# Optimization experiments

Hardware: AMD Instinct MI355X
Metric: run time of the kernel (lower is better)

Reference implementation:

```python
import jax, jax.numpy as jnp
import numpy as np

B, L, CH = 8, 32768, 128   # segments, points per segment, channels
H, D = 4, 32               # num_head, ch_head (CH == H*D)
EPS = 1e-5                 # torch GroupNorm default eps


def group_norm1(x, w, b):
    # GroupNorm(num_groups=1, num_channels=CH) applied on [1, CH, L] per segment:
    # normalize over all channels AND points of each segment, then per-channel affine.
    mu = jnp.mean(x, axis=(1, 2), keepdims=True)            # [B,1,1]
    var = jnp.var(x, axis=(1, 2), keepdims=True)            # [B,1,1]
    return (x - mu) * jax.lax.rsqrt(var + EPS) * w + b      # [B,L,CH]


def setup_inputs() -> dict:
    key = jax.random.key(0)
    k0, k1, k2 = jax.random.split(key, 3)
    x = jax.random.normal(k0, (B, L, CH), dtype=jnp.float32)
    W_qkv = jax.random.normal(k1, (CH, 3 * H * D), dtype=jnp.float32) * 0.02
    W_out = jax.random.normal(k2, (H * D, CH), dtype=jnp.float32) * 0.02
    gn1_w = jnp.ones((CH,), jnp.float32)
    gn1_b = jnp.zeros((CH,), jnp.float32)
    gn2_w = jnp.ones((CH,), jnp.float32)
    gn2_b = jnp.zeros((CH,), jnp.float32)
    return {"x": x, "gn1_w": gn1_w, "gn1_b": gn1_b, "W_qkv": W_qkv,
            "W_out": W_out, "gn2_w": gn2_w, "gn2_b": gn2_b}


def reference(x, gn1_w, gn1_b, W_qkv, W_out, gn2_w, gn2_b):
    norm_x = group_norm1(x, gn1_w, gn1_b)                     # [B,L,CH]
    qkv = norm_x @ W_qkv                                      # [B,L,3*H*D]
    q, k, v = jnp.split(qkv, 3, axis=-1)
    q = q.reshape(B, L, H, D)
    k = k.reshape(B, L, H, D)
    v = v.reshape(B, L, H, D)
    # softmax over points within each segment (k / sqrt(segment_len))
    k_soft = jax.nn.softmax(k * (1.0 / np.float32(np.sqrt(L))), axis=1)
    # per-segment, per-head KV context: [B,H,D,D]
    context = jnp.einsum('blhk,blhv->bhkv', k_soft, v)
    # q scaled by ch_head**-0.5, softmax over feature dim
    q_soft = jax.nn.softmax(q * np.float32(D ** -0.5), axis=-1)
    out = jnp.einsum('blhk,bhkv->blhv', q_soft, context).reshape(B, L, H * D)
    out = out @ W_out                                          # [B,L,CH]
    out = group_norm1(out, gn2_w, gn2_b)
    return out + x  # residual
```

## Files before the change

### kernel.cpp

```cpp
#include <hip/hip_runtime.h>

#define NSEG 8
#define LSEG 32768
#define NCH 128
#define EPS_GN 1e-5f
#define KSCALE 0.005524271728019903f
#define QSCALE 0.17677669529663687f

typedef __attribute__((ext_vector_type(4))) float f32x4;
typedef __attribute__((ext_vector_type(8))) __bf16 bf16x8;
typedef __attribute__((ext_vector_type(4))) short s16x4;

static __device__ __forceinline__ unsigned short f2bf(float f) {
  unsigned int u = __float_as_uint(f);
  u += 0x7fffu + ((u >> 16) & 1u);
  return (unsigned short)(u >> 16);
}
static __device__ __forceinline__ float bf2f(unsigned short s) {
  return __uint_as_float(((unsigned int)s) << 16);
}

__global__ void k_wcvt(const float* __restrict__ W, unsigned short* __restrict__ WT) {
  int idx = blockIdx.x * 256 + threadIdx.x;
  int n = idx >> 7, k = idx & 127;
  WT[idx] = f2bf(W[k * 384 + n]);
}

__global__ __launch_bounds__(256) void k_stats1(const float* __restrict__ x, float* __restrict__ part) {
  int t = threadIdx.x;
  int b = blockIdx.x >> 6, p = blockIdx.x & 63;
  const float4* xp = (const float4*)x + (size_t)b * 1048576 + (size_t)p * 16384;
  float s = 0.f, q = 0.f;
  for (int i = 0; i < 64; ++i) {
    float4 v = xp[t + i * 256];
    s += v.x + v.y + v.z + v.w;
    q += v.x*v.x + v.y*v.y + v.z*v.z + v.w*v.w;
  }
  #pragma unroll
  for (int o = 1; o < 64; o <<= 1) { s += __shfl_xor(s, o); q += __shfl_xor(q, o); }
  __shared__ float red[8];
  int wave = t >> 6, lane = t & 63;
  if (lane == 0) { red[wave*2] = s; red[wave*2+1] = q; }
  __syncthreads();
  if (t == 0) {
    part[blockIdx.x*2]   = red[0] + red[2] + red[4] + red[6];
    part[blockIdx.x*2+1] = red[1] + red[3] + red[5] + red[7];
  }
}

__global__ void k_stats1_final(const float* __restrict__ part, float* __restrict__ stats) {
  int b = blockIdx.x, t = threadIdx.x;
  float s = part[(b*64 + t)*2], q = part[(b*64 + t)*2 + 1];
  #pragma unroll
  for (int o = 1; o < 64; o <<= 1) { s += __shfl_xor(s, o); q += __shfl_xor(q, o); }
  if (t == 0) {
    const float invN = 1.f / 4194304.f;
    float mu = s * invN;
    float var = q * invN - mu * mu;
    stats[b*2] = mu;
    stats[b*2+1] = rsqrtf(var + EPS_GN);
  }
}

__global__ __launch_bounds__(512) void k_qkv(
    const float* __restrict__ x, const float* __restrict__ gn1w, const float* __restrict__ gn1b,
    const float* __restrict__ stats1, const unsigned short* __restrict__ WT,
    unsigned short* __restrict__ q_ws, float* __restrict__ sume_p, float* __restrict__ ctx_p)
{
  __shared__ __attribute__((aligned(16))) unsigned short sW[384 * 136];
  __shared__ __attribute__((aligned(16))) unsigned short sA[128 * 136];
  __shared__ float sume_lds[8 * 128];

  const int t = threadIdx.x;
  const int wave = t >> 6, lane = t & 63;
  const int b = blockIdx.x >> 5, sub = blockIdx.x & 31;
  const int lm = lane & 15, lg = lane >> 4;

  const ushort4* wt4 = (const ushort4*)WT;
  #pragma unroll
  for (int i = 0; i < 24; ++i) {
    int f = t + i * 512;
    *(ushort4*)&sW[(f >> 5) * 136 + (f & 31) * 4] = wt4[f];
  }

  const float mu = stats1[b*2], rs = stats1[b*2+1];
  const int c4 = t & 31;
  const float4 w4 = *(const float4*)&gn1w[c4*4];
  const float4 g4 = *(const float4*)&gn1b[c4*4];

  f32x4 ctx[4][2][2];
  #pragma unroll
  for (int h = 0; h < 4; ++h)
    #pragma unroll
    for (int i = 0; i < 2; ++i)
      #pragma unroll
      for (int j = 0; j < 2; ++j) ctx[h][i][j] = (f32x4){0.f,0.f,0.f,0.f};
  float se[8] = {0.f,0.f,0.f,0.f,0.f,0.f,0.f,0.f};

  const float4* xp = (const float4*)x + ((size_t)b * LSEG + (size_t)sub * 1024) * 32;
  ushort4* q4 = (ushort4*)q_ws;

  for (int ch = 0; ch < 8; ++ch) {
    #pragma unroll
    for (int i = 0; i < 8; ++i) {
      int f = t + i * 512;
      int row = f >> 5;
      float4 v = xp[ch * 4096 + f];
      float4 nv;
      nv.x = (v.x - mu) * rs * w4.x + g4.x;
      nv.y = (v.y - mu) * rs * w4.y + g4.y;
      nv.z = (v.z - mu) * rs * w4.z + g4.z;
      nv.w = (v.w - mu) * rs * w4.w + g4.w;
      *(ushort4*)&sA[row * 136 + c4 * 4] = make_ushort4(f2bf(nv.x), f2bf(nv.y), f2bf(nv.z), f2bf(nv.w));
    }
    __syncthreads();

    const int arow = wave * 16 + lm;
    bf16x8 af[4];
    #pragma unroll
    for (int kk = 0; kk < 4; ++kk)
      af[kk] = *(const bf16x8*)&sA[arow * 136 + kk * 32 + lg * 8];

    f32x4 qa[8];
    #pragma unroll
    for (int nt = 0; nt < 8; ++nt) qa[nt] = (f32x4){0.f,0.f,0.f,0.f};
    #pragma unroll
    for (int kk = 0; kk < 4; ++kk)
      #pragma unroll
      for (int nt = 0; nt < 8; ++nt) {
        bf16x8 bf = *(const bf16x8*)&sW[(nt * 16 + lm) * 136 + kk * 32 + lg * 8];
        qa[nt] = __builtin_amdgcn_mfma_f32_16x16x32_bf16(af[kk], bf, qa[nt], 0, 0, 0);
      }
    const size_t qbase = (((size_t)blockIdx.x * 8 + ch) * 8 + wave) * 8;
    #pragma unroll
    for (int nt = 0; nt < 8; ++nt)
      q4[(qbase + nt) * 64 + lane] =
          make_ushort4(f2bf(qa[nt][0]), f2bf(qa[nt][1]), f2bf(qa[nt][2]), f2bf(qa[nt][3]));

    f32x4 ka[8], va[8];
    #pragma unroll
    for (int j = 0; j < 8; ++j) { ka[j] = (f32x4){0.f,0.f,0.f,0.f}; va[j] = (f32x4){0.f,0.f,0.f,0.f}; }
    #pragma unroll
    for (int kk = 0; kk < 4; ++kk) {
      #pragma unroll
      for (int j = 0; j < 8; ++j) {
        bf16x8 bk = *(const bf16x8*)&sW[((8 + j) * 16 + lm) * 136 + kk * 32 + lg * 8];
        ka[j] = __builtin_amdgcn_mfma_f32_16x16x32_bf16(af[kk], bk, ka[j], 0, 0, 0);
      }
      #pragma unroll
      for (int j = 0; j < 8; ++j) {
        bf16x8 bv = *(const bf16x8*)&sW[((16 + j) * 16 + lm) * 136 + kk * 32 + lg * 8];
        va[j] = __builtin_amdgcn_mfma_f32_16x16x32_bf16(af[kk], bv, va[j], 0, 0, 0);
      }
    }
    #pragma unroll
    for (int j = 0; j < 8; ++j) {
      #pragma unroll
      for (int r = 0; r < 4; ++r) ka[j][r] = __expf(ka[j][r] * KSCALE);
      float s = ka[j][0] + ka[j][1] + ka[j][2] + ka[j][3];
      s += __shfl_xor(s, 16);
      s += __shfl_xor(s, 32);
      se[j] += s;
    }
    #pragma unroll
    for (int h = 0; h < 4; ++h) {
      s16x4 aE[2], bV[2];
      #pragma unroll
      for (int d = 0; d < 2; ++d) {
        #pragma unroll
        for (int r = 0; r < 4; ++r) {
          aE[d][r] = (short)f2bf(ka[2*h + d][r]);
          bV[d][r] = (short)f2bf(va[2*h + d][r]);
        }
      }
      #pragma unroll
      for (int dt = 0; dt < 2; ++dt)
        #pragma unroll
        for (int vt = 0; vt < 2; ++vt)
          ctx[h][dt][vt] = __builtin_amdgcn_mfma_f32_16x16x16bf16_1k(aE[dt], bV[vt], ctx[h][dt][vt], 0, 0, 0);
    }
    __syncthreads();
  }

  if (lane < 16) {
    #pragma unroll
    for (int j = 0; j < 8; ++j) sume_lds[wave * 128 + j * 16 + lane] = se[j];
  }
  __syncthreads();
  if (t < 128) {
    float s = 0.f;
    #pragma unroll
    for (int w = 0; w < 8; ++w) s += sume_lds[w * 128 + t];
    sume_p[(size_t)blockIdx.x * 128 + t] = s;
  }
  float* cbuf = (float*)sA;
  for (int w = 0; w < 8; ++w) {
    if (wave == w) {
      #pragma unroll
      for (int h = 0; h < 4; ++h)
        #pragma unroll
        for (int dt = 0; dt < 2; ++dt)
          #pragma unroll
          for (int vt = 0; vt < 2; ++vt)
            #pragma unroll
            for (int r = 0; r < 4; ++r) {
              int idx = (h * 32 + dt * 16 + lg * 4 + r) * 32 + vt * 16 + lm;
              if (w == 0) cbuf[idx] = ctx[h][dt][vt][r];
              else        cbuf[idx] += ctx[h][dt][vt][r];
            }
    }
    __syncthreads();
  }
  #pragma unroll
  for (int i = 0; i < 8; ++i) {
    int f = t + i * 512;
    ctx_p[(size_t)blockIdx.x * 4096 + f] = cbuf[f];
  }
}

__global__ __launch_bounds__(512) void k_ctx_final(
    const float* __restrict__ sume_p, const float* __restrict__ ctx_p,
    const float* __restrict__ Wout, unsigned short* __restrict__ WcT)
{
  __shared__ float sse[128];
  __shared__ float sctx[4096];
  __shared__ float sWo[16384];
  const int t = threadIdx.x, b = blockIdx.x;
  if (t < 128) {
    float s = 0.f;
    for (int blk = 0; blk < 32; ++blk) s += sume_p[(size_t)(b * 32 + blk) * 128 + t];
    sse[t] = s;
  }
  float cv[8];
  #pragma unroll
  for (int j = 0; j < 8; ++j) {
    int idx = t + j * 512;
    float s = 0.f;
    for (int blk = 0; blk < 32; ++blk) s += ctx_p[(size_t)(b * 32 + blk) * 4096 + idx];
    cv[j] = s;
  }
  #pragma unroll
  for (int j = 0; j < 32; ++j) sWo[t + j * 512] = Wout[t + j * 512];
  __syncthreads();
  #pragma unroll
  for (int j = 0; j < 8; ++j) {
    int idx = t + j * 512;
    sctx[idx] = cv[j] / sse[idx >> 5];
  }
  __syncthreads();
  const int p = t >> 2, c0 = (t & 3) * 32;
  const int h = p >> 5;
  float acc[32];
  #pragma unroll
  for (int j = 0; j < 32; ++j) acc[j] = 0.f;
  for (int v = 0; v < 32; ++v) {
    float a = sctx[p * 32 + v];
    const float* wr = &sWo[(h * 32 + v) * 128 + c0];
    #pragma unroll
    for (int j = 0; j < 32; ++j) acc[j] += a * wr[j];
  }
  #pragma unroll
  for (int j = 0; j < 32; ++j)
    WcT[((size_t)b * 128 + (c0 + j)) * 128 + p] = f2bf(acc[j]);
}

__global__ __launch_bounds__(512) void k_out(
    unsigned short* __restrict__ q_ws, const unsigned short* __restrict__ WcT,
    float* __restrict__ stats2_p)
{
  __shared__ __attribute__((aligned(16))) unsigned short sQ[128 * 136];
  __shared__ __attribute__((aligned(16))) unsigned short sWc[128 * 136];
  __shared__ __attribute__((aligned(16))) unsigned short sO[128 * 136];
  __shared__ float red[16];

  const int t = threadIdx.x;
  const int wave = t >> 6, lane = t & 63;
  const int b = blockIdx.x >> 5, sub = blockIdx.x & 31;
  const int lm = lane & 15, lg = lane >> 4;

  const ushort4* wc4 = (const ushort4*)WcT + (size_t)b * 4096;
  #pragma unroll
  for (int i = 0; i < 8; ++i) {
    int f = t + i * 512;
    *(ushort4*)&sWc[(f >> 5) * 136 + (f & 31) * 4] = wc4[f];
  }

  ushort4* q4 = (ushort4*)q_ws;
  float ssum = 0.f, ssq = 0.f;

  for (int ch = 0; ch < 8; ++ch) {
    const size_t qbase = (((size_t)blockIdx.x * 8 + ch) * 8 + wave) * 8;
    ushort4 qf[8];
    #pragma unroll
    for (int nt = 0; nt < 8; ++nt) qf[nt] = q4[(qbase + nt) * 64 + lane];
    const int rbase = wave * 16 + lg * 4;
    #pragma unroll
    for (int h = 0; h < 4; ++h) {
      float a0[4], a1[4], m[4], e0[4], e1[4], sm[4];
      a0[0] = bf2f(qf[2*h].x) * QSCALE;   a0[1] = bf2f(qf[2*h].y) * QSCALE;
      a0[2] = bf2f(qf[2*h].z) * QSCALE;   a0[3] = bf2f(qf[2*h].w) * QSCALE;
      a1[0] = bf2f(qf[2*h+1].x) * QSCALE; a1[1] = bf2f(qf[2*h+1].y) * QSCALE;
      a1[2] = bf2f(qf[2*h+1].z) * QSCALE; a1[3] = bf2f(qf[2*h+1].w) * QSCALE;
      #pragma unroll
      for (int r = 0; r < 4; ++r) m[r] = fmaxf(a0[r], a1[r]);
      #pragma unroll
      for (int o = 1; o < 16; o <<= 1)
        #pragma unroll
        for (int r = 0; r < 4; ++r) m[r] = fmaxf(m[r], __shfl_xor(m[r], o));
      #pragma unroll
      for (int r = 0; r < 4; ++r) {
        e0[r] = __expf(a0[r] - m[r]); e1[r] = __expf(a1[r] - m[r]); sm[r] = e0[r] + e1[r];
      }
      #pragma unroll
      for (int o = 1; o < 16; o <<= 1)
        #pragma unroll
        for (int r = 0; r < 4; ++r) sm[r] += __shfl_xor(sm[r], o);
      #pragma unroll
      for (int r = 0; r < 4; ++r) {
        float inv = 1.f / sm[r];
        sQ[(rbase + r) * 136 + h * 32 + lm]      = f2bf(e0[r] * inv);
        sQ[(rbase + r) * 136 + h * 32 + 16 + lm] = f2bf(e1[r] * inv);
      }
    }
    __syncthreads();
    const int arow = wave * 16 + lm;
    bf16x8 af[4];
    #pragma unroll
    for (int kk = 0; kk < 4; ++kk)
      af[kk] = *(const bf16x8*)&sQ[arow * 136 + kk * 32 + lg * 8];
    f32x4 acc[8];
    #pragma unroll
    for (int nt = 0; nt < 8; ++nt) acc[nt] = (f32x4){0.f,0.f,0.f,0.f};
    #pragma unroll
    for (int kk = 0; kk < 4; ++kk)
      #pragma unroll
      for (int nt = 0; nt < 8; ++nt) {
        bf16x8 bf = *(const bf16x8*)&sWc[(nt * 16 + lm) * 136 + kk * 32 + lg * 8];
        acc[nt] = __builtin_amdgcn_mfma_f32_16x16x32_bf16(af[kk], bf, acc[nt], 0, 0, 0);
      }
    #pragma unroll
    for (int nt = 0; nt < 8; ++nt)
      #pragma unroll
      for (int r = 0; r < 4; ++r) {
        float v = acc[nt][r];
        ssum += v; ssq += v * v;
        sO[(rbase + r) * 136 + nt * 16 + lm] = f2bf(v);
      }
    __syncthreads();
    const size_t rowg = (size_t)b * LSEG + (size_t)sub * 1024 + (size_t)ch * 128;
    #pragma unroll
    for (int i = 0; i < 8; ++i) {
      int f = t + i * 512;
      q4[(rowg + (f >> 5)) * 32 + (f & 31)] = *(const ushort4*)&sO[(f >> 5) * 136 + (f & 31) * 4];
    }
  }
  #pragma unroll
  for (int o = 1; o < 64; o <<= 1) { ssum += __shfl_xor(ssum, o); ssq += __shfl_xor(ssq, o); }
  if (lane == 0) { red[wave*2] = ssum; red[wave*2+1] = ssq; }
  __syncthreads();
  if (t == 0) {
    float s = 0.f, q = 0.f;
    #pragma unroll
    for (int w = 0; w < 8; ++w) { s += red[w*2]; q += red[w*2+1]; }
    stats2_p[blockIdx.x*2] = s; stats2_p[blockIdx.x*2+1] = q;
  }
}

__global__ void k_stats2_final(const float* __restrict__ part, float* __restrict__ stats) {
  int b = blockIdx.x, t = threadIdx.x;
  float s = part[(b*32 + t)*2], q = part[(b*32 + t)*2 + 1];
  #pragma unroll
  for (int o = 1; o < 32; o <<= 1) { s += __shfl_xor(s, o); q += __shfl_xor(q, o); }
  if (t == 0) {
    const float invN = 1.f / 4194304.f;
    float mu = s * invN;
    float var = q * invN - mu * mu;
    stats[b*2] = mu;
    stats[b*2+1] = rsqrtf(var + EPS_GN);
  }
}

__global__ __launch_bounds__(256) void k_final(
    const float* __restrict__ x, const unsigned short* __restrict__ out_ws,
    const float* __restrict__ stats2, const float* __restrict__ gn2w, const float* __restrict__ gn2b,
    float* __restrict__ y)
{
  const int t = threadIdx.x;
  const int b = blockIdx.x >> 8, blk = blockIdx.x & 255;
  const float mu = stats2[b*2], rs = stats2[b*2+1];
  const int c4 = t & 31;
  const float4 w4 = *(const float4*)&gn2w[c4*4];
  const float4 g4 = *(const float4*)&gn2b[c4*4];
  const size_t base = (size_t)b * 1048576 + (size_t)blk * 4096;
  const float4* xp = (const float4*)x + base;
  const ushort4* op = (const ushort4*)out_ws + base;
  float4* yp = (float4*)y + base;
  #pragma unroll
  for (int i = 0; i < 16; ++i) {
    int f = t + i * 256;
    float4 xv = xp[f];
    ushort4 ov = op[f];
    float4 r;
    r.x = (bf2f(ov.x) - mu) * rs * w4.x + g4.x + xv.x;
    r.y = (bf2f(ov.y) - mu) * rs * w4.y + g4.y + xv.y;
    r.z = (bf2f(ov.z) - mu) * rs * w4.z + g4.z + xv.z;
    r.w = (bf2f(ov.w) - mu) * rs * w4.w + g4.w + xv.w;
    yp[f] = r;
  }
}

extern "C" void kernel_launch(void* const* d_in, const int* in_sizes, int n_in,
                              void* d_out, int out_size, void* d_ws, size_t ws_size,
                              hipStream_t stream) {
  const float* x    = (const float*)d_in[0];
  const float* gn1w = (const float*)d_in[1];
  const float* gn1b = (const float*)d_in[2];
  const float* Wqkv = (const float*)d_in[3];
  const float* Wout = (const float*)d_in[4];
  const float* gn2w = (const float*)d_in[5];
  const float* gn2b = (const float*)d_in[6];
  float* y = (float*)d_out;
  char* ws = (char*)d_ws;

  float*          stats1p = (float*)(ws + 0);
  float*          stats1  = (float*)(ws + 4096);
  unsigned short* WT      = (unsigned short*)(ws + 8192);
  float*          sume_p  = (float*)(ws + 106496);
  float*          ctx_p   = (float*)(ws + 237568);
  unsigned short* WcT     = (unsigned short*)(ws + 4431872);
  float*          stats2p = (float*)(ws + 4694016);
  float*          stats2  = (float*)(ws + 4696064);
  unsigned short* q_ws    = (unsigned short*)(ws + 4718592);

  hipLaunchKernelGGL(k_wcvt,         dim3(192),  dim3(256), 0, stream, Wqkv, WT);
  hipLaunchKernelGGL(k_stats1,       dim3(512),  dim3(256), 0, stream, x, stats1p);
  hipLaunchKernelGGL(k_stats1_final, dim3(8),    dim3(64),  0, stream, stats1p, stats1);
  hipLaunchKernelGGL(k_qkv,          dim3(256),  dim3(512), 0, stream, x, gn1w, gn1b, stats1, WT, q_ws, sume_p, ctx_p);
  hipLaunchKernelGGL(k_ctx_final,    dim3(8),    dim3(512), 0, stream, sume_p, ctx_p, Wout, WcT);
  hipLaunchKernelGGL(k_out,          dim3(256),  dim3(512), 0, stream, q_ws, WcT, stats2p);
  hipLaunchKernelGGL(k_stats2_final, dim3(8),    dim3(32),  0, stream, stats2p, stats2);
  hipLaunchKernelGGL(k_final,        dim3(2048), dim3(256), 0, stream, x, q_ws, stats2, gn2w, gn2b, y);
}
```

Baseline: 238.1 us.

## Fold GroupNorm1 into QKV weights and bias, restructure qkv and out kernels

```diff
diff --git a/kernel.cpp b/kernel.cpp
--- a/kernel.cpp
+++ b/kernel.cpp
@@ -2,7 +2,6 @@
 
 #define NSEG 8
 #define LSEG 32768
-#define NCH 128
 #define EPS_GN 1e-5f
 #define KSCALE 0.005524271728019903f
 #define QSCALE 0.17677669529663687f
@@ -19,11 +18,28 @@
 static __device__ __forceinline__ float bf2f(unsigned short s) {
   return __uint_as_float(((unsigned int)s) << 16);
 }
-
-__global__ void k_wcvt(const float* __restrict__ W, unsigned short* __restrict__ WT) {
+static __device__ __forceinline__ bf16x8 cvt8(float4 a, float4 b) {
+  bf16x8 r;
+  r[0] = (__bf16)a.x; r[1] = (__bf16)a.y; r[2] = (__bf16)a.z; r[3] = (__bf16)a.w;
+  r[4] = (__bf16)b.x; r[5] = (__bf16)b.y; r[6] = (__bf16)b.z; r[7] = (__bf16)b.w;
+  return r;
+}
+static __device__ __forceinline__ s16x4 pack4(float a, float b, float c, float d) {
+  union { __bf16 h[4]; s16x4 s; } u;
+  u.h[0] = (__bf16)a; u.h[1] = (__bf16)b; u.h[2] = (__bf16)c; u.h[3] = (__bf16)d;
+  return u.s;
+}
+static __device__ __forceinline__ ushort4 packu4(f32x4 v) {
+  union { __bf16 h[4]; ushort4 u; } u;
+  u.h[0] = (__bf16)v[0]; u.h[1] = (__bf16)v[1]; u.h[2] = (__bf16)v[2]; u.h[3] = (__bf16)v[3];
+  return u.u;
+}
+
+__global__ void k_wcvt(const float* __restrict__ W, const float* __restrict__ gn1w,
+                       unsigned short* __restrict__ WT) {
   int idx = blockIdx.x * 256 + threadIdx.x;
-  int n = idx >> 7, k = idx & 127;
-  WT[idx] = f2bf(W[k * 384 + n]);
+  int n = idx >> 7, ch = idx & 127;
+  WT[idx] = f2bf(gn1w[ch] * W[ch * 384 + n]);
 }
 
 __global__ __launch_bounds__(256) void k_stats1(const float* __restrict__ x, float* __restrict__ part) {
@@ -62,159 +78,152 @@
   }
 }
 
-__global__ __launch_bounds__(512) void k_qkv(
-    const float* __restrict__ x, const float* __restrict__ gn1w, const float* __restrict__ gn1b,
-    const float* __restrict__ stats1, const unsigned short* __restrict__ WT,
+__global__ void k_bias(const float* __restrict__ Wqkv, const float* __restrict__ gn1w,
+                       const float* __restrict__ gn1b, const float* __restrict__ stats1,
+                       float* __restrict__ biasv, float* __restrict__ alpha) {
+  int seg = blockIdx.x, n = threadIdx.x;
+  float mu = stats1[seg*2], rs = stats1[seg*2+1];
+  float s = 0.f;
+  for (int ch = 0; ch < 128; ++ch)
+    s += (gn1b[ch] - mu * rs * gn1w[ch]) * Wqkv[ch * 384 + n];
+  float scale = (n < 128) ? QSCALE : ((n < 256) ? KSCALE : 1.f);
+  biasv[seg*384 + n] = s * scale;
+  if (n == 0) {
+    alpha[seg*4]   = rs * QSCALE;
+    alpha[seg*4+1] = rs * KSCALE;
+    alpha[seg*4+2] = rs;
+  }
+}
+
+__global__ __launch_bounds__(512, 2) void k_qkv(
+    const float* __restrict__ x, const unsigned short* __restrict__ WT,
+    const float* __restrict__ biasv, const float* __restrict__ alpha,
     unsigned short* __restrict__ q_ws, float* __restrict__ sume_p, float* __restrict__ ctx_p)
 {
-  __shared__ __attribute__((aligned(16))) unsigned short sW[384 * 136];
-  __shared__ __attribute__((aligned(16))) unsigned short sA[128 * 136];
-  __shared__ float sume_lds[8 * 128];
+  __shared__ float cbuf[4096];
+  __shared__ float sume_lds[256];
 
   const int t = threadIdx.x;
   const int wave = t >> 6, lane = t & 63;
-  const int b = blockIdx.x >> 5, sub = blockIdx.x & 31;
+  const int rg = wave >> 2, h = wave & 3;
   const int lm = lane & 15, lg = lane >> 4;
-
-  const ushort4* wt4 = (const ushort4*)WT;
-  #pragma unroll
-  for (int i = 0; i < 24; ++i) {
-    int f = t + i * 512;
-    *(ushort4*)&sW[(f >> 5) * 136 + (f & 31) * 4] = wt4[f];
-  }
-
-  const float mu = stats1[b*2], rs = stats1[b*2+1];
-  const int c4 = t & 31;
-  const float4 w4 = *(const float4*)&gn1w[c4*4];
-  const float4 g4 = *(const float4*)&gn1b[c4*4];
-
-  f32x4 ctx[4][2][2];
-  #pragma unroll
-  for (int h = 0; h < 4; ++h)
-    #pragma unroll
-    for (int i = 0; i < 2; ++i)
-      #pragma unroll
-      for (int j = 0; j < 2; ++j) ctx[h][i][j] = (f32x4){0.f,0.f,0.f,0.f};
-  float se[8] = {0.f,0.f,0.f,0.f,0.f,0.f,0.f,0.f};
-
-  const float4* xp = (const float4*)x + ((size_t)b * LSEG + (size_t)sub * 1024) * 32;
+  const int bid = blockIdx.x;
+  const int seg = bid >> 5, sub = bid & 31;
+
+  bf16x8 wq[2][4], wk[2][4], wv[2][4];
+  #pragma unroll
+  for (int nt = 0; nt < 2; ++nt)
+    #pragma unroll
+    for (int kk = 0; kk < 4; ++kk) {
+      int row = h*32 + nt*16 + lm;
+      wq[nt][kk] = *(const bf16x8*)&WT[(row      ) * 128 + kk*32 + lg*8];
+      wk[nt][kk] = *(const bf16x8*)&WT[(row + 128) * 128 + kk*32 + lg*8];
+      wv[nt][kk] = *(const bf16x8*)&WT[(row + 256) * 128 + kk*32 + lg*8];
+    }
+  const float alk = alpha[seg*4 + 1];
+  const float alv = alpha[seg*4 + 2];
+  float ckv[2], cvv[2];
+  #pragma unroll
+  for (int nt = 0; nt < 2; ++nt) {
+    ckv[nt] = biasv[seg*384 + 128 + h*32 + nt*16 + lm];
+    cvv[nt] = biasv[seg*384 + 256 + h*32 + nt*16 + lm];
+  }
+
+  f32x4 ctx00 = {0,0,0,0}, ctx01 = {0,0,0,0}, ctx10 = {0,0,0,0}, ctx11 = {0,0,0,0};
+  float se0 = 0.f, se1 = 0.f;
+
+  const float* xw = x + ((size_t)seg * LSEG + sub*1024 + rg*64 + lm) * 128 + lg*8;
   ushort4* q4 = (ushort4*)q_ws;
 
-  for (int ch = 0; ch < 8; ++ch) {
-    #pragma unroll
-    for (int i = 0; i < 8; ++i) {
-      int f = t + i * 512;
-      int row = f >> 5;
-      float4 v = xp[ch * 4096 + f];
-      float4 nv;
-      nv.x = (v.x - mu) * rs * w4.x + g4.x;
-      nv.y = (v.y - mu) * rs * w4.y + g4.y;
-      nv.z = (v.z - mu) * rs * w4.z + g4.z;
-      nv.w = (v.w - mu) * rs * w4.w + g4.w;
-      *(ushort4*)&sA[row * 136 + c4 * 4] = make_ushort4(f2bf(nv.x), f2bf(nv.y), f2bf(nv.z), f2bf(nv.w));
+#define ISSUE(S, IT) { \
+    const float* p_ = xw + (size_t)((((IT) >> 2) * 128) + (((IT) & 3) * 16)) * 128; \
+    _Pragma("unroll") \
+    for (int kk = 0; kk < 4; ++kk) { \
+      S[kk][0] = *(const float4*)(p_ + kk*32); \
+      S[kk][1] = *(const float4*)(p_ + kk*32 + 4); \
+    } }
+
+#define COMPUTE(S, IT) { \
+    bf16x8 axf[4]; \
+    _Pragma("unroll") for (int kk = 0; kk < 4; ++kk) axf[kk] = cvt8(S[kk][0], S[kk][1]); \
+    f32x4 qa0 = {0,0,0,0}, qa1 = {0,0,0,0}; \
+    _Pragma("unroll") for (int kk = 0; kk < 4; ++kk) { \
+      qa0 = __builtin_amdgcn_mfma_f32_16x16x32_bf16(wq[0][kk], axf[kk], qa0, 0, 0, 0); \
+      qa1 = __builtin_amdgcn_mfma_f32_16x16x32_bf16(wq[1][kk], axf[kk], qa1, 0, 0, 0); \
+    } \
+    { size_t T_ = ((size_t)bid*8 + ((IT) >> 2)) * 64 + (rg*4 + ((IT) & 3)) * 8 + h*2; \
+      q4[(T_    ) * 64 + lane] = packu4(qa0); \
+      q4[(T_ + 1) * 64 + lane] = packu4(qa1); } \
+    f32x4 ka0 = {0,0,0,0}, ka1 = {0,0,0,0}; \
+    _Pragma("unroll") for (int kk = 0; kk < 4; ++kk) { \
+      ka0 = __builtin_amdgcn_mfma_f32_16x16x32_bf16(axf[kk], wk[0][kk], ka0, 0, 0, 0); \
+      ka1 = __builtin_amdgcn_mfma_f32_16x16x32_bf16(axf[kk], wk[1][kk], ka1, 0, 0, 0); \
+    } \
+    f32x4 va0 = {0,0,0,0}, va1 = {0,0,0,0}; \
+    _Pragma("unroll") for (int kk = 0; kk < 4; ++kk) { \
+      va0 = __builtin_amdgcn_mfma_f32_16x16x32_bf16(axf[kk], wv[0][kk], va0, 0, 0, 0); \
+      va1 = __builtin_amdgcn_mfma_f32_16x16x32_bf16(axf[kk], wv[1][kk], va1, 0, 0, 0); \
+    } \
+    float e_[8]; \
+    _Pragma("unroll") for (int r = 0; r < 4; ++r) e_[r]     = __expf(fmaf(ka0[r], alk, ckv[0])); \
+    _Pragma("unroll") for (int r = 0; r < 4; ++r) e_[4 + r] = __expf(fmaf(ka1[r], alk, ckv[1])); \
+    se0 += (e_[0] + e_[1]) + (e_[2] + e_[3]); \
+    se1 += (e_[4] + e_[5]) + (e_[6] + e_[7]); \
+    s16x4 E0 = pack4(e_[0], e_[1], e_[2], e_[3]); \
+    s16x4 E1 = pack4(e_[4], e_[5], e_[6], e_[7]); \
+    s16x4 V0 = pack4(fmaf(va0[0], alv, cvv[0]), fmaf(va0[1], alv, cvv[0]), \
+                     fmaf(va0[2], alv, cvv[0]), fmaf(va0[3], alv, cvv[0])); \
+    s16x4 V1 = pack4(fmaf(va1[0], alv, cvv[1]), fmaf(va1[1], alv, cvv[1]), \
+                     fmaf(va1[2], alv, cvv[1]), fmaf(va1[3], alv, cvv[1])); \
+    ctx00 = __builtin_amdgcn_mfma_f32_16x16x16bf16_1k(E0, V0, ctx00, 0, 0, 0); \
+    ctx01 = __builtin_amdgcn_mfma_f32_16x16x16bf16_1k(E0, V1, ctx01, 0, 0, 0); \
+    ctx10 = __builtin_amdgcn_mfma_f32_16x16x16bf16_1k(E1, V0, ctx10, 0, 0, 0); \
+    ctx11 = __builtin_amdgcn_mfma_f32_16x16x16bf16_1k(E1, V1, ctx11, 0, 0, 0); \
+  }
+
+  float4 pa[4][2], pb[4][2];
+  ISSUE(pa, 0);
+  #pragma unroll 1
+  for (int it = 0; it < 32; it += 2) {
+    ISSUE(pb, it + 1);
+    COMPUTE(pa, it);
+    if (it + 2 < 32) ISSUE(pa, it + 2);
+    COMPUTE(pb, it + 1);
+  }
+#undef ISSUE
+#undef COMPUTE
+
+  se0 += __shfl_xor(se0, 16); se0 += __shfl_xor(se0, 32);
+  se1 += __shfl_xor(se1, 16); se1 += __shfl_xor(se1, 32);
+  if (lane < 16) {
+    sume_lds[rg*128 + h*32 + lm]      = se0;
+    sume_lds[rg*128 + h*32 + 16 + lm] = se1;
+  }
+  if (rg == 0) {
+    #pragma unroll
+    for (int r = 0; r < 4; ++r) {
+      cbuf[h*1024 + (lg*4 + r)*32      + lm]      = ctx00[r];
+      cbuf[h*1024 + (lg*4 + r)*32      + 16 + lm] = ctx01[r];
+      cbuf[h*1024 + (16 + lg*4 + r)*32 + lm]      = ctx10[r];
+      cbuf[h*1024 + (16 + lg*4 + r)*32 + 16 + lm] = ctx11[r];
     }
-    __syncthreads();
-
-    const int arow = wave * 16 + lm;
-    bf16x8 af[4];
-    #pragma unroll
-    for (int kk = 0; kk < 4; ++kk)
-      af[kk] = *(const bf16x8*)&sA[arow * 136 + kk * 32 + lg * 8];
-
-    f32x4 qa[8];
-    #pragma unroll
-    for (int nt = 0; nt < 8; ++nt) qa[nt] = (f32x4){0.f,0.f,0.f,0.f};
-    #pragma unroll
-    for (int kk = 0; kk < 4; ++kk)
-      #pragma unroll
-      for (int nt = 0; nt < 8; ++nt) {
-        bf16x8 bf = *(const bf16x8*)&sW[(nt * 16 + lm) * 136 + kk * 32 + lg * 8];
-        qa[nt] = __builtin_amdgcn_mfma_f32_16x16x32_bf16(af[kk], bf, qa[nt], 0, 0, 0);
-      }
-    const size_t qbase = (((size_t)blockIdx.x * 8 + ch) * 8 + wave) * 8;
-    #pragma unroll
-    for (int nt = 0; nt < 8; ++nt)
-      q4[(qbase + nt) * 64 + lane] =
-          make_ushort4(f2bf(qa[nt][0]), f2bf(qa[nt][1]), f2bf(qa[nt][2]), f2bf(qa[nt][3]));
-
-    f32x4 ka[8], va[8];
-    #pragma unroll
-    for (int j = 0; j < 8; ++j) { ka[j] = (f32x4){0.f,0.f,0.f,0.f}; va[j] = (f32x4){0.f,0.f,0.f,0.f}; }
-    #pragma unroll
-    for (int kk = 0; kk < 4; ++kk) {
-      #pragma unroll
-      for (int j = 0; j < 8; ++j) {
-        bf16x8 bk = *(const bf16x8*)&sW[((8 + j) * 16 + lm) * 136 + kk * 32 + lg * 8];
-        ka[j] = __builtin_amdgcn_mfma_f32_16x16x32_bf16(af[kk], bk, ka[j], 0, 0, 0);
-      }
-      #pragma unroll
-      for (int j = 0; j < 8; ++j) {
-        bf16x8 bv = *(const bf16x8*)&sW[((16 + j) * 16 + lm) * 136 + kk * 32 + lg * 8];
-        va[j] = __builtin_amdgcn_mfma_f32_16x16x32_bf16(af[kk], bv, va[j], 0, 0, 0);
-      }
+  }
+  __syncthreads();
+  if (rg == 1) {
+    #pragma unroll
+    for (int r = 0; r < 4; ++r) {
+      cbuf[h*1024 + (lg*4 + r)*32      + lm]      += ctx00[r];
+      cbuf[h*1024 + (lg*4 + r)*32      + 16 + lm] += ctx01[r];
+      cbuf[h*1024 + (16 + lg*4 + r)*32 + lm]      += ctx10[r];
+      cbuf[h*1024 + (16 + lg*4 + r)*32 + 16 + lm] += ctx11[r];
     }
-    #pragma unroll
-    for (int j = 0; j < 8; ++j) {
-      #pragma unroll
-      for (int r = 0; r < 4; ++r) ka[j][r] = __expf(ka[j][r] * KSCALE);
-      float s = ka[j][0] + ka[j][1] + ka[j][2] + ka[j][3];
-      s += __shfl_xor(s, 16);
-      s += __shfl_xor(s, 32);
-      se[j] += s;
-    }
-    #pragma unroll
-    for (int h = 0; h < 4; ++h) {
-      s16x4 aE[2], bV[2];
-      #pragma unroll
-      for (int d = 0; d < 2; ++d) {
-        #pragma unroll
-        for (int r = 0; r < 4; ++r) {
-          aE[d][r] = (short)f2bf(ka[2*h + d][r]);
-          bV[d][r] = (short)f2bf(va[2*h + d][r]);
-        }
-      }
-      #pragma unroll
-      for (int dt = 0; dt < 2; ++dt)
-        #pragma unroll
-        for (int vt = 0; vt < 2; ++vt)
-          ctx[h][dt][vt] = __builtin_amdgcn_mfma_f32_16x16x16bf16_1k(aE[dt], bV[vt], ctx[h][dt][vt], 0, 0, 0);
-    }
-    __syncthreads();
-  }
-
-  if (lane < 16) {
-    #pragma unroll
-    for (int j = 0; j < 8; ++j) sume_lds[wave * 128 + j * 16 + lane] = se[j];
-  }
-  __syncthreads();
-  if (t < 128) {
-    float s = 0.f;
-    #pragma unroll
-    for (int w = 0; w < 8; ++w) s += sume_lds[w * 128 + t];
-    sume_p[(size_t)blockIdx.x * 128 + t] = s;
-  }
-  float* cbuf = (float*)sA;
-  for (int w = 0; w < 8; ++w) {
-    if (wave == w) {
-      #pragma unroll
-      for (int h = 0; h < 4; ++h)
-        #pragma unroll
-        for (int dt = 0; dt < 2; ++dt)
-          #pragma unroll
-          for (int vt = 0; vt < 2; ++vt)
-            #pragma unroll
-            for (int r = 0; r < 4; ++r) {
-              int idx = (h * 32 + dt * 16 + lg * 4 + r) * 32 + vt * 16 + lm;
-              if (w == 0) cbuf[idx] = ctx[h][dt][vt][r];
-              else        cbuf[idx] += ctx[h][dt][vt][r];
-            }
-    }
-    __syncthreads();
-  }
+  }
+  __syncthreads();
+  if (t < 128) sume_p[(size_t)bid*128 + t] = sume_lds[t] + sume_lds[128 + t];
   #pragma unroll
   for (int i = 0; i < 8; ++i) {
     int f = t + i * 512;
-    ctx_p[(size_t)blockIdx.x * 4096 + f] = cbuf[f];
+    ctx_p[(size_t)bid*4096 + f] = cbuf[f];
   }
 }
 
@@ -266,94 +275,86 @@
 
 __global__ __launch_bounds__(512) void k_out(
     unsigned short* __restrict__ q_ws, const unsigned short* __restrict__ WcT,
+    const float* __restrict__ biasv, const float* __restrict__ alpha,
     float* __restrict__ stats2_p)
 {
-  __shared__ __attribute__((aligned(16))) unsigned short sQ[128 * 136];
   __shared__ __attribute__((aligned(16))) unsigned short sWc[128 * 136];
-  __shared__ __attribute__((aligned(16))) unsigned short sO[128 * 136];
+  __shared__ __attribute__((aligned(16))) unsigned char sO[8][16 * 272];
   __shared__ float red[16];
 
-  const int t = threadIdx.x;
-  const int wave = t >> 6, lane = t & 63;
-  const int b = blockIdx.x >> 5, sub = blockIdx.x & 31;
+  const int t = threadIdx.x, wave = t >> 6, lane = t & 63;
   const int lm = lane & 15, lg = lane >> 4;
-
-  const ushort4* wc4 = (const ushort4*)WcT + (size_t)b * 4096;
+  const int bid = blockIdx.x;
+  const int seg = bid >> 8;
+
+  const ushort4* q4c = (const ushort4*)q_ws;
+  ushort4 qt[8];
+  #pragma unroll
+  for (int kt = 0; kt < 8; ++kt)
+    qt[kt] = q4c[((size_t)bid * 64 + wave * 8 + kt) * 64 + lane];
+
+  const ushort4* wc4 = (const ushort4*)WcT + (size_t)seg * 4096;
   #pragma unroll
   for (int i = 0; i < 8; ++i) {
     int f = t + i * 512;
     *(ushort4*)&sWc[(f >> 5) * 136 + (f & 31) * 4] = wc4[f];
   }
-
-  ushort4* q4 = (ushort4*)q_ws;
+  const float alq = alpha[seg * 4];
+  float4 cq[8];
+  #pragma unroll
+  for (int kt = 0; kt < 8; ++kt)
+    cq[kt] = *(const float4*)&biasv[seg * 384 + kt * 16 + lg * 4];
+
+  __syncthreads();
+
+  s16x4 p[8];
+  #pragma unroll
+  for (int h = 0; h < 4; ++h) {
+    float a[8];
+    #pragma unroll
+    for (int nt = 0; nt < 2; ++nt) {
+      const unsigned short* qe = (const unsigned short*)&qt[2*h + nt];
+      const float* cqe = (const float*)&cq[2*h + nt];
+      #pragma unroll
+      for (int r = 0; r < 4; ++r)
+        a[nt*4 + r] = fmaf(bf2f(qe[r]), alq, cqe[r]);
+    }
+    float m = a[0];
+    #pragma unroll
+    for (int i = 1; i < 8; ++i) m = fmaxf(m, a[i]);
+    m = fmaxf(m, __shfl_xor(m, 16));
+    m = fmaxf(m, __shfl_xor(m, 32));
+    float s = 0.f;
+    #pragma unroll
+    for (int i = 0; i < 8; ++i) { a[i] = __expf(a[i] - m); s += a[i]; }
+    s += __shfl_xor(s, 16);
+    s += __shfl_xor(s, 32);
+    float inv = 1.f / s;
+    p[2*h]   = pack4(a[0]*inv, a[1]*inv, a[2]*inv, a[3]*inv);
+    p[2*h+1] = pack4(a[4]*inv, a[5]*inv, a[6]*inv, a[7]*inv);
+  }
+
   float ssum = 0.f, ssq = 0.f;
-
-  for (int ch = 0; ch < 8; ++ch) {
-    const size_t qbase = (((size_t)blockIdx.x * 8 + ch) * 8 + wave) * 8;
-    ushort4 qf[8];
-    #pragma unroll
-    for (int nt = 0; nt < 8; ++nt) qf[nt] = q4[(qbase + nt) * 64 + lane];
-    const int rbase = wave * 16 + lg * 4;
-    #pragma unroll
-    for (int h = 0; h < 4; ++h) {
-      float a0[4], a1[4], m[4], e0[4], e1[4], sm[4];
-      a0[0] = bf2f(qf[2*h].x) * QSCALE;   a0[1] = bf2f(qf[2*h].y) * QSCALE;
-      a0[2] = bf2f(qf[2*h].z) * QSCALE;   a0[3] = bf2f(qf[2*h].w) * QSCALE;
-      a1[0] = bf2f(qf[2*h+1].x) * QSCALE; a1[1] = bf2f(qf[2*h+1].y) * QSCALE;
-      a1[2] = bf2f(qf[2*h+1].z) * QSCALE; a1[3] = bf2f(qf[2*h+1].w) * QSCALE;
-      #pragma unroll
-      for (int r = 0; r < 4; ++r) m[r] = fmaxf(a0[r], a1[r]);
-      #pragma unroll
-      for (int o = 1; o < 16; o <<= 1)
-        #pragma unroll
-        for (int r = 0; r < 4; ++r) m[r] = fmaxf(m[r], __shfl_xor(m[r], o));
-      #pragma unroll
-      for (int r = 0; r < 4; ++r) {
-        e0[r] = __expf(a0[r] - m[r]); e1[r] = __expf(a1[r] - m[r]); sm[r] = e0[r] + e1[r];
-      }
-      #pragma unroll
-      for (int o = 1; o < 16; o <<= 1)
-        #pragma unroll
-        for (int r = 0; r < 4; ++r) sm[r] += __shfl_xor(sm[r], o);
-      #pragma unroll
-      for (int r = 0; r < 4; ++r) {
-        float inv = 1.f / sm[r];
-        sQ[(rbase + r) * 136 + h * 32 + lm]      = f2bf(e0[r] * inv);
-        sQ[(rbase + r) * 136 + h * 32 + 16 + lm] = f2bf(e1[r] * inv);
-      }
+  unsigned char* so = &sO[wave][0];
+  #pragma unroll
+  for (int ot = 0; ot < 8; ++ot) {
+    f32x4 acc = {0,0,0,0};
+    #pragma unroll
+    for (int kt = 0; kt < 8; ++kt) {
+      s16x4 wf = *(const s16x4*)&sWc[(ot*16 + lm) * 136 + kt*16 + lg*4];
+      acc = __builtin_amdgcn_mfma_f32_16x16x16bf16_1k(wf, p[kt], acc, 0, 0, 0);
     }
-    __syncthreads();
-    const int arow = wave * 16 + lm;
-    bf16x8 af[4];
-    #pragma unroll
-    for (int kk = 0; kk < 4; ++kk)
-      af[kk] = *(const bf16x8*)&sQ[arow * 136 + kk * 32 + lg * 8];
-    f32x4 acc[8];
-    #pragma unroll
-    for (int nt = 0; nt < 8; ++nt) acc[nt] = (f32x4){0.f,0.f,0.f,0.f};
-    #pragma unroll
-    for (int kk = 0; kk < 4; ++kk)
-      #pragma unroll
-      for (int nt = 0; nt < 8; ++nt) {
-        bf16x8 bf = *(const bf16x8*)&sWc[(nt * 16 + lm) * 136 + kk * 32 + lg * 8];
-        acc[nt] = __builtin_amdgcn_mfma_f32_16x16x32_bf16(af[kk], bf, acc[nt], 0, 0, 0);
-      }
-    #pragma unroll
-    for (int nt = 0; nt < 8; ++nt)
-      #pragma unroll
-      for (int r = 0; r < 4; ++r) {
-        float v = acc[nt][r];
-        ssum += v; ssq += v * v;
-        sO[(rbase + r) * 136 + nt * 16 + lm] = f2bf(v);
-      }
-    __syncthreads();
-    const size_t rowg = (size_t)b * LSEG + (size_t)sub * 1024 + (size_t)ch * 128;
-    #pragma unroll
-    for (int i = 0; i < 8; ++i) {
-      int f = t + i * 512;
-      q4[(rowg + (f >> 5)) * 32 + (f & 31)] = *(const ushort4*)&sO[(f >> 5) * 136 + (f & 31) * 4];
-    }
-  }
+    #pragma unroll
+    for (int r = 0; r < 4; ++r) { ssum += acc[r]; ssq += acc[r] * acc[r]; }
+    *(ushort4*)(so + lm * 272 + ot * 32 + lg * 8) = packu4(acc);
+  }
+  #pragma unroll
+  for (int i = 0; i < 4; ++i) {
+    int row = i * 4 + (lane >> 4);
+    float4 v = *(const float4*)(so + row * 272 + (lane & 15) * 16);
+    *(float4*)((char*)q_ws + ((size_t)bid * 128 + wave * 16 + row) * 256 + (lane & 15) * 16) = v;
+  }
+
   #pragma unroll
   for (int o = 1; o < 64; o <<= 1) { ssum += __shfl_xor(ssum, o); ssq += __shfl_xor(ssq, o); }
   if (lane == 0) { red[wave*2] = ssum; red[wave*2+1] = ssq; }
@@ -362,19 +363,25 @@
     float s = 0.f, q = 0.f;
     #pragma unroll
     for (int w = 0; w < 8; ++w) { s += red[w*2]; q += red[w*2+1]; }
-    stats2_p[blockIdx.x*2] = s; stats2_p[blockIdx.x*2+1] = q;
+    stats2_p[bid*2] = s; stats2_p[bid*2+1] = q;
   }
 }
 
 __global__ void k_stats2_final(const float* __restrict__ part, float* __restrict__ stats) {
   int b = blockIdx.x, t = threadIdx.x;
-  float s = part[(b*32 + t)*2], q = part[(b*32 + t)*2 + 1];
-  #pragma unroll
-  for (int o = 1; o < 32; o <<= 1) { s += __shfl_xor(s, o); q += __shfl_xor(q, o); }
+  float s = part[(b*256 + t)*2], q = part[(b*256 + t)*2 + 1];
+  #pragma unroll
+  for (int o = 1; o < 64; o <<= 1) { s += __shfl_xor(s, o); q += __shfl_xor(q, o); }
+  __shared__ float red[8];
+  int wave = t >> 6, lane = t & 63;
+  if (lane == 0) { red[wave*2] = s; red[wave*2+1] = q; }
+  __syncthreads();
   if (t == 0) {
+    float ss = red[0] + red[2] + red[4] + red[6];
+    float qq = red[1] + red[3] + red[5] + red[7];
     const float invN = 1.f / 4194304.f;
-    float mu = s * invN;
-    float var = q * invN - mu * mu;
+    float mu = ss * invN;
+    float var = qq * invN - mu * mu;
     stats[b*2] = mu;
     stats[b*2+1] = rsqrtf(var + EPS_GN);
   }
@@ -425,19 +432,22 @@
   float*          stats1p = (float*)(ws + 0);
   float*          stats1  = (float*)(ws + 4096);
   unsigned short* WT      = (unsigned short*)(ws + 8192);
-  float*          sume_p  = (float*)(ws + 106496);
-  float*          ctx_p   = (float*)(ws + 237568);
-  unsigned short* WcT     = (unsigned short*)(ws + 4431872);
-  float*          stats2p = (float*)(ws + 4694016);
-  float*          stats2  = (float*)(ws + 4696064);
-  unsigned short* q_ws    = (unsigned short*)(ws + 4718592);
-
-  hipLaunchKernelGGL(k_wcvt,         dim3(192),  dim3(256), 0, stream, Wqkv, WT);
+  float*          biasv   = (float*)(ws + 106496);
+  float*          alphav  = (float*)(ws + 118784);
+  float*          sume_p  = (float*)(ws + 122880);
+  float*          ctx_p   = (float*)(ws + 253952);
+  unsigned short* WcT     = (unsigned short*)(ws + 4448256);
+  float*          stats2p = (float*)(ws + 4710400);
+  float*          stats2  = (float*)(ws + 4726784);
+  unsigned short* q_ws    = (unsigned short*)(ws + 4849664);
+
+  hipLaunchKernelGGL(k_wcvt,         dim3(192),  dim3(256), 0, stream, Wqkv, gn1w, WT);
   hipLaunchKernelGGL(k_stats1,       dim3(512),  dim3(256), 0, stream, x, stats1p);
   hipLaunchKernelGGL(k_stats1_final, dim3(8),    dim3(64),  0, stream, stats1p, stats1);
-  hipLaunchKernelGGL(k_qkv,          dim3(256),  dim3(512), 0, stream, x, gn1w, gn1b, stats1, WT, q_ws, sume_p, ctx_p);
+  hipLaunchKernelGGL(k_bias,         dim3(8),    dim3(384), 0, stream, Wqkv, gn1w, gn1b, stats1, biasv, alphav);
+  hipLaunchKernelGGL(k_qkv,          dim3(256),  dim3(512), 0, stream, x, WT, biasv, alphav, q_ws, sume_p, ctx_p);
   hipLaunchKernelGGL(k_ctx_final,    dim3(8),    dim3(512), 0, stream, sume_p, ctx_p, Wout, WcT);
-  hipLaunchKernelGGL(k_out,          dim3(256),  dim3(512), 0, stream, q_ws, WcT, stats2p);
-  hipLaunchKernelGGL(k_stats2_final, dim3(8),    dim3(32),  0, stream, stats2p, stats2);
+  hipLaunchKernelGGL(k_out,          dim3(2048), dim3(512), 0, stream, q_ws, WcT, biasv, alphav, stats2p);
+  hipLaunchKernelGGL(k_stats2_final, dim3(8),    dim3(256), 0, stream, stats2p, stats2);
   hipLaunchKernelGGL(k_final,        dim3(2048), dim3(256), 0, stream, x, q_ws, stats2, gn2w, gn2b, y);
 }
```

Result: faster. 214.0 us (-10.1%).
